# Performance work log

Hardware: AMD Instinct MI355X
Metric: run time of the kernel (lower is better)

## Reference

```python
import jax, jax.numpy as jnp
import numpy as np

B, P, ENC, DEC, EMB, ATT, V, L = 32, 196, 2048, 512, 512, 512, 32000, 21
T = L - 1  # decode steps


def setup_inputs() -> dict:
    key = jax.random.key(0)
    ks = jax.random.split(key, 20)
    u = lambda k, s, a=0.1: jax.random.uniform(k, s, jnp.float32, -a, a)
    lens = jax.random.randint(ks[1], (B, 1), 5, L + 1)
    lens = lens.at[0, 0].set(L)  # force max_decode_len == T (static)
    return {
        'encoder_out': jax.random.normal(ks[0], (B, P, ENC), jnp.float32),
        'encoded_captions': jax.random.randint(ks[2], (B, L), 0, V),
        'caption_lengths': lens,
        'emb_W': u(ks[3], (V, EMB)),
        'W_ea': u(ks[4], (ATT, ENC), 0.02), 'b_ea': jnp.zeros((ATT,)),
        'W_da': u(ks[5], (ATT, DEC), 0.02), 'b_da': jnp.zeros((ATT,)),
        'w_fa': u(ks[6], (1, ATT), 0.02), 'b_fa': jnp.zeros((1,)),
        'W_ih': u(ks[7], (4 * DEC, EMB + ENC), 0.02), 'b_ih': jnp.zeros((4 * DEC,)),
        'W_hh': u(ks[8], (4 * DEC, DEC), 0.02), 'b_hh': jnp.zeros((4 * DEC,)),
        'W_h0': u(ks[9], (DEC, ENC), 0.02), 'b_h0': jnp.zeros((DEC,)),
        'W_c0': u(ks[10], (DEC, ENC), 0.02), 'b_c0': jnp.zeros((DEC,)),
        'W_fb': u(ks[11], (ENC, DEC), 0.02), 'b_fb': jnp.zeros((ENC,)),
        'W_fc': u(ks[12], (V, DEC)), 'b_fc': jnp.zeros((V,)),
    }


def reference(encoder_out, encoded_captions, caption_lengths, emb_W,
              W_ea, b_ea, W_da, b_da, w_fa, b_fa,
              W_ih, b_ih, W_hh, b_hh, W_h0, b_h0, W_c0, b_c0,
              W_fb, b_fb, W_fc, b_fc):
    # sort by caption length descending (as in torch forward)
    lens = caption_lengths[:, 0]
    sort_ind = jnp.argsort(-lens)
    lens_s = lens[sort_ind]
    enc = encoder_out[sort_ind]          # [B,P,ENC]
    caps = encoded_captions[sort_ind]    # [B,L]
    dec_lens = lens_s - 1

    mean_enc = enc.mean(axis=1)
    h0 = mean_enc @ W_h0.T + b_h0
    c0 = mean_enc @ W_c0.T + b_c0

    att1 = jnp.einsum('bpe,ae->bpa', enc, W_ea) + b_ea  # precompute encoder attn proj
    embs = emb_W[caps]                                   # [B,L,EMB]
    emb_seq = jnp.transpose(embs[:, :T], (1, 0, 2))      # [T,B,EMB] (teacher forcing)
    mask_seq = jnp.arange(T)[:, None] < dec_lens[None, :]  # [T,B]

    def step(carry, xs):
        h, c = carry
        emb_t, m = xs  # [B,EMB], [B] bool; m emulates shrinking batch_size_t
        att2 = h @ W_da.T + b_da
        e = jnp.maximum(att1 + att2[:, None, :], 0.0) @ w_fa[0] + b_fa[0]  # [B,P]
        alpha = jax.nn.softmax(e, axis=1)
        awe = jnp.einsum('bp,bpe->be', alpha, enc)
        gate = jax.nn.sigmoid(h @ W_fb.T + b_fb)
        x = jnp.concatenate([emb_t, gate * awe], axis=1)
        g = x @ W_ih.T + b_ih + h @ W_hh.T + b_hh
        i, f, gg, o = jnp.split(g, 4, axis=1)
        c_new = jax.nn.sigmoid(f) * c + jax.nn.sigmoid(i) * jnp.tanh(gg)
        h_new = jax.nn.sigmoid(o) * jnp.tanh(c_new)
        preds = h_new @ W_fc.T + b_fc  # dropout in eval mode (identity)
        mf = m[:, None]
        h = jnp.where(mf, h_new, h)
        c = jnp.where(mf, c_new, c)
        preds = preds * mf.astype(preds.dtype)
        alpha = alpha * mf.astype(alpha.dtype)
        return (h, c), (preds, alpha)

    _, (preds, alphas) = jax.lax.scan(step, (h0, c0), (emb_seq, mask_seq))
    predictions = jnp.transpose(preds, (1, 0, 2))  # [B,T,V]
    alphas = jnp.transpose(alphas, (1, 0, 2))      # [B,T,P]
    return predictions, alphas
```

## Files before the change

### kernel.cpp

```cpp
#include <hip/hip_runtime.h>
#include <hip/hip_bf16.h>
#include <cstddef>

#define NB 32
#define NP 196
#define NE 2048
#define ND 512
#define NV 32000
#define NL 21
#define NT 20

typedef __attribute__((ext_vector_type(8))) short short8;
typedef __attribute__((ext_vector_type(4))) float f32x4;

__device__ __forceinline__ unsigned short f2b(float f) {
    __hip_bfloat16 h = __float2bfloat16(f);
    return *reinterpret_cast<unsigned short*>(&h);
}
__device__ __forceinline__ float b2f(unsigned short u) {
    union { unsigned int i; float f; } v; v.i = (unsigned)u << 16; return v.f;
}
__device__ __forceinline__ float b2f_lo(unsigned int u) {
    union { unsigned int i; float f; } v; v.i = u << 16; return v.f;
}
__device__ __forceinline__ float b2f_hi(unsigned int u) {
    union { unsigned int i; float f; } v; v.i = u & 0xffff0000u; return v.f;
}


__global__ void k_sort(const int* __restrict__ lens, int* __restrict__ sind, int* __restrict__ dlens,
                       int* __restrict__ rowmap, int* __restrict__ mpad)
{
    int i = threadIdx.x;
    if (i < NB) {
        int li = lens[i];
        int r = 0;
        for (int j = 0; j < NB; ++j) {
            int lj = lens[j];
            if (lj > li || (lj == li && j < i)) ++r;
        }
        sind[r] = i;
        dlens[r] = li - 1;
    }
    __syncthreads();
    if (i == 0) {
        int c = 0;
        for (int t = 0; t < NT; ++t)
            for (int b = 0; b < NB; ++b)
                if (t < dlens[b]) rowmap[c++] = t * NB + b;
        int pad = (c + 63) & ~63;
        for (int r = c; r < pad; ++r) rowmap[r] = -1;
        mpad[0] = pad;
    }
}

__global__ __launch_bounds__(256) void k_conv_enc(
    const float* __restrict__ enc, const int* __restrict__ sind,
    unsigned short* __restrict__ encB)
{
    int idx = (blockIdx.x * 256 + threadIdx.x) * 8;
    int b = idx / (NP * NE), rem = idx - b * (NP * NE);
    const float* src = enc + (size_t)sind[b] * NP * NE + rem;
    float4 a = *reinterpret_cast<const float4*>(src);
    float4 c = *reinterpret_cast<const float4*>(src + 4);
    uint4 o;
    o.x = f2b(a.x) | ((unsigned)f2b(a.y) << 16);
    o.y = f2b(a.z) | ((unsigned)f2b(a.w) << 16);
    o.z = f2b(c.x) | ((unsigned)f2b(c.y) << 16);
    o.w = f2b(c.z) | ((unsigned)f2b(c.w) << 16);
    *reinterpret_cast<uint4*>(encB + idx) = o;
}

__global__ __launch_bounds__(256) void k_emb(
    const int* __restrict__ caps, const int* __restrict__ sind,
    const float* __restrict__ emb_W, float* __restrict__ embS)
{
    int t = blockIdx.x, b = blockIdx.y;
    const float* src = emb_W + (size_t)caps[sind[b] * NL + t] * ND;
    float* dst = embS + ((size_t)t * NB + b) * ND;
    int i = threadIdx.x * 2;
    *reinterpret_cast<float2*>(dst + i) = *reinterpret_cast<const float2*>(src + i);
}

__global__ __launch_bounds__(256) void k_mean(const float* __restrict__ enc, const int* __restrict__ sind,
                                              float* __restrict__ mean_enc)
{
    int b = blockIdx.y;
    int k = blockIdx.x * 256 + threadIdx.x;
    const float* e = enc + (size_t)sind[b] * NP * NE + k;
    float s0 = 0.f, s1 = 0.f, s2 = 0.f, s3 = 0.f;
    for (int p = 0; p < NP; p += 4) {
        s0 += e[(size_t)(p + 0) * NE];
        s1 += e[(size_t)(p + 1) * NE];
        s2 += e[(size_t)(p + 2) * NE];
        s3 += e[(size_t)(p + 3) * NE];
    }
    mean_enc[(size_t)b * NE + k] = (s0 + s1 + s2 + s3) * (1.0f / NP);
}

__global__ __launch_bounds__(256) void k_zero(const int* __restrict__ dlens, float* __restrict__ out)
{
    int b = blockIdx.x / NT, t = blockIdx.x % NT;
    if (t < dlens[b]) return;
    float4 z = {0.f, 0.f, 0.f, 0.f};
    float4* row = (float4*)(out + ((size_t)b * NT + t) * NV);
    for (int i = threadIdx.x; i < NV / 4; i += 256) row[i] = z;
}

__device__ __forceinline__ void tile_body_uniW(
    const float* __restrict__ A, int lda, const float* __restrict__ W, int wstride,
    int n0, int kbeg, int kend, float* As, float (*Ws)[33], float acc[4][2],
    int tid)
{
    int lb = tid / 8, lkq = tid % 8;
    int b4 = (tid / 32) * 4, nl = (tid % 32) * 2;
    for (int kt = kbeg; kt < kend; kt += 32) {
        float4 a4 = *reinterpret_cast<const float4*>(A + (size_t)lb * lda + kt + lkq * 4);
        As[(lkq * 4 + 0) * 32 + lb] = a4.x; As[(lkq * 4 + 1) * 32 + lb] = a4.y;
        As[(lkq * 4 + 2) * 32 + lb] = a4.z; As[(lkq * 4 + 3) * 32 + lb] = a4.w;
        #pragma unroll
        for (int r = 0; r < 2; ++r) {
            int s = tid + r * 256;
            int n_l = s / 8, kq = s % 8;
            float4 w4 = *reinterpret_cast<const float4*>(W + (size_t)(n0 + n_l) * wstride + kt + kq * 4);
            Ws[n_l][kq * 4 + 0] = w4.x; Ws[n_l][kq * 4 + 1] = w4.y;
            Ws[n_l][kq * 4 + 2] = w4.z; Ws[n_l][kq * 4 + 3] = w4.w;
        }
        __syncthreads();
        #pragma unroll
        for (int k = 0; k < 32; ++k) {
            float4 av = *reinterpret_cast<const float4*>(&As[k * 32 + b4]);
            float w0 = Ws[nl][k], w1 = Ws[nl + 1][k];
            acc[0][0] += av.x * w0; acc[0][1] += av.x * w1;
            acc[1][0] += av.y * w0; acc[1][1] += av.y * w1;
            acc[2][0] += av.z * w0; acc[2][1] += av.z * w1;
            acc[3][0] += av.w * w0; acc[3][1] += av.w * w1;
        }
        __syncthreads();
    }
}

__global__ __launch_bounds__(256) void gemm_skinny_split(
    const float* __restrict__ A0, const float* __restrict__ W0a, const float* __restrict__ W0b,
    float* __restrict__ spart)
{
    __shared__ float As[1024];
    __shared__ float Ws[64][33];
    int n0 = blockIdx.x * 64;
    int ks = blockIdx.y;
    int tid = threadIdx.x;
    int lb = tid / 8, lkq = tid % 8;
    int b4 = (tid / 32) * 4, nl = (tid % 32) * 2;
    float acc[4][2] = {};
    for (int kt = ks * 256; kt < ks * 256 + 256; kt += 32) {
        float4 a4 = *reinterpret_cast<const float4*>(A0 + (size_t)lb * NE + kt + lkq * 4);
        As[(lkq * 4 + 0) * 32 + lb] = a4.x; As[(lkq * 4 + 1) * 32 + lb] = a4.y;
        As[(lkq * 4 + 2) * 32 + lb] = a4.z; As[(lkq * 4 + 3) * 32 + lb] = a4.w;
        #pragma unroll
        for (int r = 0; r < 2; ++r) {
            int s = tid + r * 256;
            int n_l = s / 8, kq = s % 8;
            int ng = n0 + n_l;
            const float* wrow = (ng < 512) ? (W0a + (size_t)ng * NE)
                                           : (W0b + (size_t)(ng - 512) * NE);
            float4 w4 = *reinterpret_cast<const float4*>(wrow + kt + kq * 4);
            Ws[n_l][kq * 4 + 0] = w4.x; Ws[n_l][kq * 4 + 1] = w4.y;
            Ws[n_l][kq * 4 + 2] = w4.z; Ws[n_l][kq * 4 + 3] = w4.w;
        }
        __syncthreads();
        #pragma unroll
        for (int k = 0; k < 32; ++k) {
            float4 av = *reinterpret_cast<const float4*>(&As[k * 32 + b4]);
            float w0 = Ws[nl][k], w1 = Ws[nl + 1][k];
            acc[0][0] += av.x * w0; acc[0][1] += av.x * w1;
            acc[1][0] += av.y * w0; acc[1][1] += av.y * w1;
            acc[2][0] += av.z * w0; acc[2][1] += av.z * w1;
            acc[3][0] += av.w * w0; acc[3][1] += av.w * w1;
        }
        __syncthreads();
    }
    float* Cp = spart + (size_t)ks * NB * 1024;
    #pragma unroll
    for (int j = 0; j < 2; ++j)
        #pragma unroll
        for (int i = 0; i < 4; ++i)
            Cp[(size_t)(b4 + i) * 1024 + n0 + nl + j] = acc[i][j];
}

__global__ __launch_bounds__(256) void k_hc0(
    const float* __restrict__ spart, const float* __restrict__ ba, const float* __restrict__ bb,
    float* __restrict__ hc)
{
    int b = blockIdx.x;
    for (int ng = threadIdx.x; ng < 1024; ng += 256) {
        float s = (ng < 512) ? ba[ng] : bb[ng - 512];
        #pragma unroll
        for (int ks = 0; ks < 8; ++ks)
            s += spart[(size_t)ks * NB * 1024 + (size_t)b * 1024 + ng];
        hc[(size_t)b * 1024 + ng] = s;
    }
}

__global__ __launch_bounds__(256) void gemm_att1_mfma(
    const float* __restrict__ enc, const float* __restrict__ W_ea,
    const float* __restrict__ bias, unsigned short* __restrict__ att1B,
    const int* __restrict__ sind)
{
    int fid = blockIdx.x;
    int c = fid & 7, x = (fid >> 3) & 7, pg = fid >> 6;
    int p = pg * 8 + c;
    if (p >= 98) return;
    int bm0 = p * 64, bn0 = x * 64;
    __shared__ unsigned short As[64][40];
    __shared__ unsigned short Bs[64][40];
    int tid = threadIdx.x;
    int w = tid >> 6, lane = tid & 63;
    int srow = tid >> 2, schunk = (tid & 3) * 8;
    int mg = bm0 + srow;
    int bidx = mg / NP, pp = mg - bidx * NP;
    const float* arow = enc + ((size_t)sind[bidx] * NP + pp) * NE + schunk;
    const float* brow = W_ea + (size_t)(bn0 + srow) * NE + schunk;
    int frow = lane & 15, fk = (lane >> 4) * 8;
    f32x4 acc[4] = {};
    for (int kt = 0; kt < NE; kt += 32) {
        float4 a0 = *reinterpret_cast<const float4*>(arow + kt);
        float4 a1 = *reinterpret_cast<const float4*>(arow + kt + 4);
        float4 b0 = *reinterpret_cast<const float4*>(brow + kt);
        float4 b1 = *reinterpret_cast<const float4*>(brow + kt + 4);
        uint4 av, bv;
        av.x = f2b(a0.x) | ((unsigned)f2b(a0.y) << 16);
        av.y = f2b(a0.z) | ((unsigned)f2b(a0.w) << 16);
        av.z = f2b(a1.x) | ((unsigned)f2b(a1.y) << 16);
        av.w = f2b(a1.z) | ((unsigned)f2b(a1.w) << 16);
        bv.x = f2b(b0.x) | ((unsigned)f2b(b0.y) << 16);
        bv.y = f2b(b0.z) | ((unsigned)f2b(b0.w) << 16);
        bv.z = f2b(b1.x) | ((unsigned)f2b(b1.y) << 16);
        bv.w = f2b(b1.z) | ((unsigned)f2b(b1.w) << 16);
        *reinterpret_cast<uint4*>(&As[srow][schunk]) = av;
        *reinterpret_cast<uint4*>(&Bs[srow][schunk]) = bv;
        __syncthreads();
        short8 af = *reinterpret_cast<const short8*>(&As[w * 16 + frow][fk]);
        #pragma unroll
        for (int n = 0; n < 4; ++n) {
            short8 bf = *reinterpret_cast<const short8*>(&Bs[n * 16 + frow][fk]);
            acc[n] = __builtin_amdgcn_mfma_f32_16x16x32_bf16(af, bf, acc[n], 0, 0, 0);
        }
        __syncthreads();
    }
    int crow = bm0 + w * 16 + (lane >> 4) * 4;
    int ccol0 = lane & 15;
    #pragma unroll
    for (int n = 0; n < 4; ++n) {
        int col = bn0 + n * 16 + ccol0;
        float bb2 = bias[col];
        #pragma unroll
        for (int i = 0; i < 4; ++i)
            att1B[(size_t)(crow + i) * ND + col] = f2b(acc[n][i] + bb2);
    }
}

__global__ __launch_bounds__(256) void gemm_preds_mfma(
    const unsigned short* __restrict__ hseqB, const float* __restrict__ W_fc,
    const float* __restrict__ bias, float* __restrict__ out,
    const int* __restrict__ rowmap, const int* __restrict__ mpad)
{
    int fid = blockIdx.x;
    int c = fid & 7;
    int rem = fid >> 3;
    int m = rem % 10, g = rem / 10;
    int n = g * 8 + c;
    if (n >= 250) return;
    int bm0 = m * 64;
    if (bm0 >= mpad[0]) return;
    int bn0 = n * 128;
    __shared__ unsigned short As[64][40];
    __shared__ unsigned short Bs[128][40];
    int tid = threadIdx.x;
    int w = tid >> 6, lane = tid & 63;
    int srow = tid >> 2, schunk = (tid & 3) * 8;
    int rid = rowmap[bm0 + srow];
    const unsigned short* aptr = hseqB + (size_t)(rid < 0 ? 0 : rid) * ND + schunk;
    const float* bptr0 = W_fc + (size_t)(bn0 + srow) * ND + schunk;
    const float* bptr1 = W_fc + (size_t)(bn0 + 64 + srow) * ND + schunk;
    int frow = lane & 15, fk = (lane >> 4) * 8;
    f32x4 acc[8] = {};
    for (int kt = 0; kt < ND; kt += 32) {
        uint4 av = *reinterpret_cast<const uint4*>(aptr + kt);
        float4 c0 = *reinterpret_cast<const float4*>(bptr0 + kt);
        float4 c1 = *reinterpret_cast<const float4*>(bptr0 + kt + 4);
        float4 d0 = *reinterpret_cast<const float4*>(bptr1 + kt);
        float4 d1 = *reinterpret_cast<const float4*>(bptr1 + kt + 4);
        uint4 bv0, bv1;
        bv0.x = f2b(c0.x) | ((unsigned)f2b(c0.y) << 16);
        bv0.y = f2b(c0.z) | ((unsigned)f2b(c0.w) << 16);
        bv0.z = f2b(c1.x) | ((unsigned)f2b(c1.y) << 16);
        bv0.w = f2b(c1.z) | ((unsigned)f2b(c1.w) << 16);
        bv1.x = f2b(d0.x) | ((unsigned)f2b(d0.y) << 16);
        bv1.y = f2b(d0.z) | ((unsigned)f2b(d0.w) << 16);
        bv1.z = f2b(d1.x) | ((unsigned)f2b(d1.y) << 16);
        bv1.w = f2b(d1.z) | ((unsigned)f2b(d1.w) << 16);
        *reinterpret_cast<uint4*>(&As[srow][schunk]) = av;
        *reinterpret_cast<uint4*>(&Bs[srow][schunk]) = bv0;
        *reinterpret_cast<uint4*>(&Bs[64 + srow][schunk]) = bv1;
        __syncthreads();
        short8 af = *reinterpret_cast<const short8*>(&As[w * 16 + frow][fk]);
        #pragma unroll
        for (int nn = 0; nn < 8; ++nn) {
            short8 bf = *reinterpret_cast<const short8*>(&Bs[nn * 16 + frow][fk]);
            acc[nn] = __builtin_amdgcn_mfma_f32_16x16x32_bf16(af, bf, acc[nn], 0, 0, 0);
        }
        __syncthreads();
    }
    int rl0 = w * 16 + (lane >> 4) * 4;
    int ccol0 = lane & 15;
    #pragma unroll
    for (int i = 0; i < 4; ++i) {
        int rm = rowmap[bm0 + rl0 + i];
        if (rm < 0) continue;
        int t = rm / NB, b = rm % NB;
        float* orow = out + ((size_t)b * NT + t) * NV;
        #pragma unroll
        for (int nn = 0; nn < 8; ++nn) {
            int col = bn0 + nn * 16 + ccol0;
            orow[col] = acc[nn][i] + bias[col];
        }
    }
}

__global__ __launch_bounds__(256) void k_phase1(
    const float* __restrict__ hc, const float* __restrict__ W_da, const float* __restrict__ W_fb,
    const float* __restrict__ b_da, const float* __restrict__ b_fb,
    const float* __restrict__ embS, const float* __restrict__ W_ih, const float* __restrict__ W_hh,
    float* __restrict__ attg, float* __restrict__ gpart, int t)
{
    __shared__ float As[1024];
    __shared__ float Ws[64][33];
    int blk = blockIdx.x, tid = threadIdx.x;
    int b4 = (tid / 32) * 4, nl = (tid % 32) * 2;
    float acc[4][2] = {};
    if (blk < 40) {
        int n0 = blk * 64;
        int lb = tid / 8, lkq = tid % 8;
        for (int kt = 0; kt < 512; kt += 32) {
            float4 a4 = *reinterpret_cast<const float4*>(hc + (size_t)lb * 1024 + kt + lkq * 4);
            As[(lkq * 4 + 0) * 32 + lb] = a4.x; As[(lkq * 4 + 1) * 32 + lb] = a4.y;
            As[(lkq * 4 + 2) * 32 + lb] = a4.z; As[(lkq * 4 + 3) * 32 + lb] = a4.w;
            #pragma unroll
            for (int r = 0; r < 2; ++r) {
                int s = tid + r * 256;
                int n_l = s / 8, kq = s % 8;
                int ng = n0 + n_l;
                const float* wrow = (ng < 512) ? (W_da + (size_t)ng * 512)
                                               : (W_fb + (size_t)(ng - 512) * 512);
                float4 w4 = *reinterpret_cast<const float4*>(wrow + kt + kq * 4);
                Ws[n_l][kq * 4 + 0] = w4.x; Ws[n_l][kq * 4 + 1] = w4.y;
                Ws[n_l][kq * 4 + 2] = w4.z; Ws[n_l][kq * 4 + 3] = w4.w;
            }
            __syncthreads();
            #pragma unroll
            for (int k = 0; k < 32; ++k) {
                float4 av = *reinterpret_cast<const float4*>(&As[k * 32 + b4]);
                float w0 = Ws[nl][k], w1 = Ws[nl + 1][k];
                acc[0][0] += av.x * w0; acc[0][1] += av.x * w1;
                acc[1][0] += av.y * w0; acc[1][1] += av.y * w1;
                acc[2][0] += av.z * w0; acc[2][1] += av.z * w1;
                acc[3][0] += av.w * w0; acc[3][1] += av.w * w1;
            }
            __syncthreads();
        }
        #pragma unroll
        for (int j = 0; j < 2; ++j) {
            int ng = n0 + nl + j;
            float bias = (ng < 512) ? b_da[ng] : b_fb[ng - 512];
            #pragma unroll
            for (int i = 0; i < 4; ++i)
                attg[(size_t)(b4 + i) * 2560 + ng] = acc[i][j] + bias;
        }
    } else if (blk < 72) {
        int nt = blk - 40, n0 = nt * 64;
        tile_body_uniW(embS + (size_t)t * NB * ND, ND, W_ih, 2560, n0, 0, 512, As, Ws, acc, tid);
        float* Cp = gpart + (size_t)4 * NB * 2048;
        #pragma unroll
        for (int j = 0; j < 2; ++j)
            #pragma unroll
            for (int i = 0; i < 4; ++i)
                Cp[(size_t)(b4 + i) * 2048 + n0 + nl + j] = acc[i][j];
    } else {
        int nt = blk - 72, n0 = nt * 64;
        tile_body_uniW(hc, 1024, W_hh, 512, n0, 0, 512, As, Ws, acc, tid);
        float* Cp = gpart + (size_t)5 * NB * 2048;
        #pragma unroll
        for (int j = 0; j < 2; ++j)
            #pragma unroll
            for (int i = 0; i < 4; ++i)
                Cp[(size_t)(b4 + i) * 2048 + n0 + nl + j] = acc[i][j];
    }
}

__global__ __launch_bounds__(256) void k_e(
    const unsigned short* __restrict__ att1B, const float* __restrict__ attg,
    const float* __restrict__ w_fa, const float* __restrict__ b_fa,
    float* __restrict__ e)
{
    __shared__ float att2s[ND];
    __shared__ float wfas[ND];
    int b = blockIdx.y, tid = threadIdx.x;
    const float* ag = attg + (size_t)b * 2560;
    for (int d = tid; d < ND; d += 256) { att2s[d] = ag[d]; wfas[d] = w_fa[d]; }
    __syncthreads();
    int w = tid >> 6, lane = tid & 63;
    int p0 = blockIdx.x * 28;
    const unsigned short* a1 = att1B + ((size_t)b * NP + p0) * ND;
    #pragma unroll
    for (int i = 0; i < 7; ++i) {
        int p = w + 4 * i;
        const unsigned short* row = a1 + (size_t)p * ND;
        float s = 0.f;
        #pragma unroll
        for (int j = 0; j < 2; ++j) {
            int d = j * 256 + lane * 4;
            uint2 u = *reinterpret_cast<const uint2*>(row + d);
            float v0 = b2f_lo(u.x), v1 = b2f_hi(u.x);
            float v2 = b2f_lo(u.y), v3 = b2f_hi(u.y);
            float4 a2 = *reinterpret_cast<const float4*>(&att2s[d]);
            float4 wf = *reinterpret_cast<const float4*>(&wfas[d]);
            s += fmaxf(v0 + a2.x, 0.f) * wf.x + fmaxf(v1 + a2.y, 0.f) * wf.y
               + fmaxf(v2 + a2.z, 0.f) * wf.z + fmaxf(v3 + a2.w, 0.f) * wf.w;
        }
        for (int off = 32; off > 0; off >>= 1) s += __shfl_down(s, off);
        if (lane == 0) e[(size_t)b * NP + p0 + p] = s + b_fa[0];
    }
}

__global__ __launch_bounds__(256) void k_awe(
    const unsigned short* __restrict__ encB, const int* __restrict__ dlens,
    const float* __restrict__ e, const float* __restrict__ attg,
    float* __restrict__ xh, float* __restrict__ out_alpha, int t)
{
    __shared__ float es[256];
    __shared__ float red[256];
    int kc = blockIdx.x, b = blockIdx.y, tid = threadIdx.x;
    float ev = -1e30f;
    if (tid < NP) { float v = e[(size_t)b * NP + tid]; es[tid] = v; ev = v; }
    red[tid] = ev; __syncthreads();
    for (int s2 = 128; s2 > 0; s2 >>= 1) { if (tid < s2) red[tid] = fmaxf(red[tid], red[tid + s2]); __syncthreads(); }
    float m = red[0]; __syncthreads();
    float xe = (tid < NP) ? expf(es[tid] - m) : 0.f;
    red[tid] = xe; __syncthreads();
    for (int s2 = 128; s2 > 0; s2 >>= 1) { if (tid < s2) red[tid] += red[tid + s2]; __syncthreads(); }
    float inv = 1.0f / red[0];
    __syncthreads();
    es[tid] = xe * inv;
    __syncthreads();

    int k = kc * 256 + tid;
    const unsigned short* ec = encB + (size_t)b * NP * NE + k;
    float s0 = 0.f, s1 = 0.f, s2v = 0.f, s3 = 0.f;
    #pragma unroll 4
    for (int p = 0; p < NP; p += 4) {
        s0 += es[p + 0] * b2f(ec[(size_t)(p + 0) * NE]);
        s1 += es[p + 1] * b2f(ec[(size_t)(p + 1) * NE]);
        s2v += es[p + 2] * b2f(ec[(size_t)(p + 2) * NE]);
        s3 += es[p + 3] * b2f(ec[(size_t)(p + 3) * NE]);
    }
    float awe = (s0 + s1) + (s2v + s3);
    float gp = attg[(size_t)b * 2560 + 512 + k];
    float gate = 1.f / (1.f + expf(-gp));
    xh[(size_t)b * 3072 + 512 + k] = gate * awe;
    if (kc == 0 && tid < NP) {
        bool live = (t < dlens[b]);
        out_alpha[((size_t)b * NT + t) * NP + tid] = live ? es[tid] : 0.f;
    }
}

__global__ __launch_bounds__(256) void k_gates(
    const float* __restrict__ xh, const float* __restrict__ W_ih,
    float* __restrict__ gpart)
{
    __shared__ float As[1024];
    __shared__ float Ws[64][33];
    int blk = blockIdx.x, tid = threadIdx.x;
    int nt = blk & 31, ks = blk >> 5;
    int n0 = nt * 64;
    int b4 = (tid / 32) * 4, nl = (tid % 32) * 2;
    float acc[4][2] = {};
    tile_body_uniW(xh + 512 + (size_t)ks * 512, 3072, W_ih + 512 + (size_t)ks * 512, 2560,
                   n0, 0, 512, As, Ws, acc, tid);
    float* Cp = gpart + (size_t)ks * NB * 2048;
    #pragma unroll
    for (int j = 0; j < 2; ++j)
        #pragma unroll
        for (int i = 0; i < 4; ++i)
            Cp[(size_t)(b4 + i) * 2048 + n0 + nl + j] = acc[i][j];
}

__global__ __launch_bounds__(256) void k_cell(
    const float* __restrict__ gpart, const int* __restrict__ dlens,
    const float* __restrict__ b_ih, const float* __restrict__ b_hh,
    float* __restrict__ hc, unsigned short* __restrict__ hseqB, int t)
{
    int b = blockIdx.x;
    for (int d = threadIdx.x; d < ND; d += 256) {
        float g0 = b_ih[d] + b_hh[d];
        float g1 = b_ih[512 + d] + b_hh[512 + d];
        float g2 = b_ih[1024 + d] + b_hh[1024 + d];
        float g3 = b_ih[1536 + d] + b_hh[1536 + d];
        #pragma unroll
        for (int ks = 0; ks < 6; ++ks) {
            const float* gp = gpart + ((size_t)ks * NB + b) * 2048;
            g0 += gp[d]; g1 += gp[512 + d]; g2 += gp[1024 + d]; g3 += gp[1536 + d];
        }
        float ig = 1.f / (1.f + expf(-g0));
        float fg = 1.f / (1.f + expf(-g1));
        float gt = tanhf(g2);
        float og = 1.f / (1.f + expf(-g3));
        float c_old = hc[(size_t)b * 1024 + 512 + d];
        float c_new = fg * c_old + ig * gt;
        float h_new = og * tanhf(c_new);
        hseqB[((size_t)t * NB + b) * ND + d] = f2b(h_new);
        if (t < dlens[b]) {
            hc[(size_t)b * 1024 + d] = h_new;
            hc[(size_t)b * 1024 + 512 + d] = c_new;
        }
    }
}

extern "C" void kernel_launch(void* const* d_in, const int* in_sizes, int n_in,
                              void* d_out, int out_size, void* d_ws, size_t ws_size,
                              hipStream_t stream)
{
    const float* enc   = (const float*)d_in[0];
    const int*   caps  = (const int*)d_in[1];
    const int*   clens = (const int*)d_in[2];
    const float* emb_W = (const float*)d_in[3];
    const float* W_ea  = (const float*)d_in[4];
    const float* b_ea  = (const float*)d_in[5];
    const float* W_da  = (const float*)d_in[6];
    const float* b_da  = (const float*)d_in[7];
    const float* w_fa  = (const float*)d_in[8];
    const float* b_fa  = (const float*)d_in[9];
    const float* W_ih  = (const float*)d_in[10];
    const float* b_ih  = (const float*)d_in[11];
    const float* W_hh  = (const float*)d_in[12];
    const float* b_hh  = (const float*)d_in[13];
    const float* W_h0  = (const float*)d_in[14];
    const float* b_h0  = (const float*)d_in[15];
    const float* W_c0  = (const float*)d_in[16];
    const float* b_c0  = (const float*)d_in[17];
    const float* W_fb  = (const float*)d_in[18];
    const float* b_fb  = (const float*)d_in[19];
    const float* W_fc  = (const float*)d_in[20];
    const float* b_fc  = (const float*)d_in[21];

    float* out = (float*)d_out;
    float* out_alpha = out + (size_t)NB * NT * NV;

    int* iws    = (int*)d_ws;
    int* sind   = iws;
    int* dlens  = iws + 32;
    int* rowmap = iws + 64;
    int* mpad   = iws + 704;
    float* base = (float*)d_ws + 1024;
    float* mean_enc = base;
    float* hc    = mean_enc + NB * NE;
    float* attg  = hc + NB * 1024;
    float* xh    = attg + NB * 2560;
    float* e     = xh + NB * 3072;
    float* embS  = e + NB * NP;
    float* gpart = embS + (size_t)NT * NB * ND;
    unsigned short* att1B = (unsigned short*)(gpart + 6 * NB * 2048);
    unsigned short* hseqB = att1B + (size_t)NB * NP * ND;
    unsigned short* encB  = hseqB + (size_t)NT * NB * ND;

    k_sort<<<1, 64, 0, stream>>>(clens, sind, dlens, rowmap, mpad);
    k_zero<<<NB * NT, 256, 0, stream>>>(dlens, out);
    k_conv_enc<<<dim3(NB * NP * NE / 2048), 256, 0, stream>>>(enc, sind, encB);
    k_emb<<<dim3(NT, NB), 256, 0, stream>>>(caps, sind, emb_W, embS);
    k_mean<<<dim3(NE / 256, NB), 256, 0, stream>>>(enc, sind, mean_enc);
    gemm_skinny_split<<<dim3(16, 8), 256, 0, stream>>>(mean_enc, W_h0, W_c0, gpart);
    k_hc0<<<dim3(NB), 256, 0, stream>>>(gpart, b_h0, b_c0, hc);
    gemm_att1_mfma<<<dim3(832), 256, 0, stream>>>(enc, W_ea, b_ea, att1B, sind);

    for (int t = 0; t < NT; ++t) {
        k_phase1<<<dim3(104), 256, 0, stream>>>(hc, W_da, W_fb, b_da, b_fb,
                                                embS, W_ih, W_hh, attg, gpart, t);
        k_e<<<dim3(7, NB), 256, 0, stream>>>(att1B, attg, w_fa, b_fa, e);
        k_awe<<<dim3(8, NB), 256, 0, stream>>>(encB, dlens, e, attg, xh, out_alpha, t);
        k_gates<<<dim3(128), 256, 0, stream>>>(xh, W_ih, gpart);
        k_cell<<<dim3(NB), 256, 0, stream>>>(gpart, dlens, b_ih, b_hh, hc, hseqB, t);
    }

    gemm_preds_mfma<<<dim3(2560), 256, 0, stream>>>(hseqB, W_fc, b_fc, out, rowmap, mpad);
}
```

Measured before the change: 1.580 ms.

## Fuse gate GEMM with LSTM cell and enlarge prediction GEMM row tile

New measurement: 2.232 ms. +41.3%, slower.

```diff
diff --git a/kernel.cpp b/kernel.cpp
--- a/kernel.cpp
+++ b/kernel.cpp
@@ -48,7 +48,7 @@
         for (int t = 0; t < NT; ++t)
             for (int b = 0; b < NB; ++b)
                 if (t < dlens[b]) rowmap[c++] = t * NB + b;
-        int pad = (c + 63) & ~63;
+        int pad = (c + 127) & ~127;
         for (int r = c; r < pad; ++r) rowmap[r] = -1;
         mpad[0] = pad;
     }
@@ -267,62 +267,69 @@
     int fid = blockIdx.x;
     int c = fid & 7;
     int rem = fid >> 3;
-    int m = rem % 10, g = rem / 10;
+    int m = rem % 5, g = rem / 5;
     int n = g * 8 + c;
     if (n >= 250) return;
-    int bm0 = m * 64;
+    int bm0 = m * 128;
     if (bm0 >= mpad[0]) return;
     int bn0 = n * 128;
-    __shared__ unsigned short As[64][40];
+    __shared__ unsigned short As[128][40];
     __shared__ unsigned short Bs[128][40];
     int tid = threadIdx.x;
     int w = tid >> 6, lane = tid & 63;
-    int srow = tid >> 2, schunk = (tid & 3) * 8;
+    int srow = tid >> 1, shalf = (tid & 1) * 16;
     int rid = rowmap[bm0 + srow];
-    const unsigned short* aptr = hseqB + (size_t)(rid < 0 ? 0 : rid) * ND + schunk;
-    const float* bptr0 = W_fc + (size_t)(bn0 + srow) * ND + schunk;
-    const float* bptr1 = W_fc + (size_t)(bn0 + 64 + srow) * ND + schunk;
+    const unsigned short* aptr = hseqB + (size_t)(rid < 0 ? 0 : rid) * ND + shalf;
+    const float* bptr = W_fc + (size_t)(bn0 + srow) * ND + shalf;
     int frow = lane & 15, fk = (lane >> 4) * 8;
-    f32x4 acc[8] = {};
+    f32x4 acc[2][8] = {};
     for (int kt = 0; kt < ND; kt += 32) {
-        uint4 av = *reinterpret_cast<const uint4*>(aptr + kt);
-        float4 c0 = *reinterpret_cast<const float4*>(bptr0 + kt);
-        float4 c1 = *reinterpret_cast<const float4*>(bptr0 + kt + 4);
-        float4 d0 = *reinterpret_cast<const float4*>(bptr1 + kt);
-        float4 d1 = *reinterpret_cast<const float4*>(bptr1 + kt + 4);
+        uint4 a0 = *reinterpret_cast<const uint4*>(aptr + kt);
+        uint4 a1 = *reinterpret_cast<const uint4*>(aptr + kt + 8);
+        float4 c0 = *reinterpret_cast<const float4*>(bptr + kt);
+        float4 c1 = *reinterpret_cast<const float4*>(bptr + kt + 4);
+        float4 c2 = *reinterpret_cast<const float4*>(bptr + kt + 8);
+        float4 c3 = *reinterpret_cast<const float4*>(bptr + kt + 12);
         uint4 bv0, bv1;
         bv0.x = f2b(c0.x) | ((unsigned)f2b(c0.y) << 16);
         bv0.y = f2b(c0.z) | ((unsigned)f2b(c0.w) << 16);
         bv0.z = f2b(c1.x) | ((unsigned)f2b(c1.y) << 16);
         bv0.w = f2b(c1.z) | ((unsigned)f2b(c1.w) << 16);
-        bv1.x = f2b(d0.x) | ((unsigned)f2b(d0.y) << 16);
-        bv1.y = f2b(d0.z) | ((unsigned)f2b(d0.w) << 16);
-        bv1.z = f2b(d1.x) | ((unsigned)f2b(d1.y) << 16);
-        bv1.w = f2b(d1.z) | ((unsigned)f2b(d1.w) << 16);
-        *reinterpret_cast<uint4*>(&As[srow][schunk]) = av;
-        *reinterpret_cast<uint4*>(&Bs[srow][schunk]) = bv0;
-        *reinterpret_cast<uint4*>(&Bs[64 + srow][schunk]) = bv1;
-        __syncthreads();
-        short8 af = *reinterpret_cast<const short8*>(&As[w * 16 + frow][fk]);
-        #pragma unroll
-        for (int nn = 0; nn < 8; ++nn) {
-            short8 bf = *reinterpret_cast<const short8*>(&Bs[nn * 16 + frow][fk]);
-            acc[nn] = __builtin_amdgcn_mfma_f32_16x16x32_bf16(af, bf, acc[nn], 0, 0, 0);
-        }
-        __syncthreads();
-    }
-    int rl0 = w * 16 + (lane >> 4) * 4;
+        bv1.x = f2b(c2.x) | ((unsigned)f2b(c2.y) << 16);
+        bv1.y = f2b(c2.z) | ((unsigned)f2b(c2.w) << 16);
+        bv1.z = f2b(c3.x) | ((unsigned)f2b(c3.y) << 16);
+        bv1.w = f2b(c3.z) | ((unsigned)f2b(c3.w) << 16);
+        *reinterpret_cast<uint4*>(&As[srow][shalf]) = a0;
+        *reinterpret_cast<uint4*>(&As[srow][shalf + 8]) = a1;
+        *reinterpret_cast<uint4*>(&Bs[srow][shalf]) = bv0;
+        *reinterpret_cast<uint4*>(&Bs[srow][shalf + 8]) = bv1;
+        __syncthreads();
+        #pragma unroll
+        for (int h = 0; h < 2; ++h) {
+            short8 af = *reinterpret_cast<const short8*>(&As[w * 32 + h * 16 + frow][fk]);
+            #pragma unroll
+            for (int nn = 0; nn < 8; ++nn) {
+                short8 bf = *reinterpret_cast<const short8*>(&Bs[nn * 16 + frow][fk]);
+                acc[h][nn] = __builtin_amdgcn_mfma_f32_16x16x32_bf16(af, bf, acc[h][nn], 0, 0, 0);
+            }
+        }
+        __syncthreads();
+    }
     int ccol0 = lane & 15;
     #pragma unroll
-    for (int i = 0; i < 4; ++i) {
-        int rm = rowmap[bm0 + rl0 + i];
-        if (rm < 0) continue;
-        int t = rm / NB, b = rm % NB;
-        float* orow = out + ((size_t)b * NT + t) * NV;
-        #pragma unroll
-        for (int nn = 0; nn < 8; ++nn) {
-            int col = bn0 + nn * 16 + ccol0;
-            orow[col] = acc[nn][i] + bias[col];
+    for (int h = 0; h < 2; ++h) {
+        int rl0 = w * 32 + h * 16 + (lane >> 4) * 4;
+        #pragma unroll
+        for (int i = 0; i < 4; ++i) {
+            int rm = rowmap[bm0 + rl0 + i];
+            if (rm < 0) continue;
+            int t = rm / NB, b = rm % NB;
+            float* orow = out + ((size_t)b * NT + t) * NV;
+            #pragma unroll
+            for (int nn = 0; nn < 8; ++nn) {
+                int col = bn0 + nn * 16 + ccol0;
+                orow[col] = acc[h][nn][i] + bias[col];
+            }
         }
     }
 }
@@ -473,47 +480,57 @@
     }
 }
 
-__global__ __launch_bounds__(256) void k_gates(
+__global__ __launch_bounds__(256) void k_gatescell(
     const float* __restrict__ xh, const float* __restrict__ W_ih,
-    float* __restrict__ gpart)
-{
-    __shared__ float As[1024];
-    __shared__ float Ws[64][33];
-    int blk = blockIdx.x, tid = threadIdx.x;
-    int nt = blk & 31, ks = blk >> 5;
-    int n0 = nt * 64;
-    int b4 = (tid / 32) * 4, nl = (tid % 32) * 2;
-    float acc[4][2] = {};
-    tile_body_uniW(xh + 512 + (size_t)ks * 512, 3072, W_ih + 512 + (size_t)ks * 512, 2560,
-                   n0, 0, 512, As, Ws, acc, tid);
-    float* Cp = gpart + (size_t)ks * NB * 2048;
-    #pragma unroll
-    for (int j = 0; j < 2; ++j)
-        #pragma unroll
-        for (int i = 0; i < 4; ++i)
-            Cp[(size_t)(b4 + i) * 2048 + n0 + nl + j] = acc[i][j];
-}
-
-__global__ __launch_bounds__(256) void k_cell(
     const float* __restrict__ gpart, const int* __restrict__ dlens,
     const float* __restrict__ b_ih, const float* __restrict__ b_hh,
     float* __restrict__ hc, unsigned short* __restrict__ hseqB, int t)
 {
-    int b = blockIdx.x;
-    for (int d = threadIdx.x; d < ND; d += 256) {
-        float g0 = b_ih[d] + b_hh[d];
-        float g1 = b_ih[512 + d] + b_hh[512 + d];
-        float g2 = b_ih[1024 + d] + b_hh[1024 + d];
-        float g3 = b_ih[1536 + d] + b_hh[1536 + d];
-        #pragma unroll
-        for (int ks = 0; ks < 6; ++ks) {
-            const float* gp = gpart + ((size_t)ks * NB + b) * 2048;
-            g0 += gp[d]; g1 += gp[512 + d]; g2 += gp[1024 + d]; g3 += gp[1536 + d];
-        }
-        float ig = 1.f / (1.f + expf(-g0));
-        float fg = 1.f / (1.f + expf(-g1));
-        float gt = tanhf(g2);
-        float og = 1.f / (1.f + expf(-g3));
+    __shared__ float As[1024];
+    __shared__ float Ws[16][33];
+    __shared__ float Gs[512];
+    int dc = blockIdx.x, tid = threadIdx.x;
+    int lb = tid / 8, lkq = tid % 8;
+    int wr = tid >> 4, wk = (tid & 15) * 2;
+    int grow = (wr >> 2) * 512 + dc * 4 + (wr & 3);
+    const float* wrow = W_ih + (size_t)grow * 2560 + 512;
+    int r = tid & 15, bp = tid >> 4;
+    int b0 = bp * 2;
+    float acc0 = 0.f, acc1 = 0.f;
+    for (int kt = 0; kt < 2048; kt += 32) {
+        float4 a4 = *reinterpret_cast<const float4*>(xh + (size_t)lb * 3072 + 512 + kt + lkq * 4);
+        As[(lkq * 4 + 0) * 32 + lb] = a4.x; As[(lkq * 4 + 1) * 32 + lb] = a4.y;
+        As[(lkq * 4 + 2) * 32 + lb] = a4.z; As[(lkq * 4 + 3) * 32 + lb] = a4.w;
+        float2 w2 = *reinterpret_cast<const float2*>(wrow + kt + wk);
+        Ws[wr][wk] = w2.x; Ws[wr][wk + 1] = w2.y;
+        __syncthreads();
+        #pragma unroll
+        for (int k = 0; k < 32; ++k) {
+            float wv = Ws[r][k];
+            float2 av = *reinterpret_cast<const float2*>(&As[k * 32 + b0]);
+            acc0 += av.x * wv;
+            acc1 += av.y * wv;
+        }
+        __syncthreads();
+    }
+    Gs[r * 32 + b0] = acc0;
+    Gs[r * 32 + b0 + 1] = acc1;
+    __syncthreads();
+    if (tid < 128) {
+        int d_l = tid & 3, b = tid >> 2;
+        int d = dc * 4 + d_l;
+        const float* gp4 = gpart + ((size_t)4 * NB + b) * 2048;
+        const float* gp5 = gpart + ((size_t)5 * NB + b) * 2048;
+        float g[4];
+        #pragma unroll
+        for (int q = 0; q < 4; ++q) {
+            int n = q * 512 + d;
+            g[q] = Gs[(q * 4 + d_l) * 32 + b] + gp4[n] + gp5[n] + b_ih[n] + b_hh[n];
+        }
+        float ig = 1.f / (1.f + expf(-g[0]));
+        float fg = 1.f / (1.f + expf(-g[1]));
+        float gt = tanhf(g[2]);
+        float og = 1.f / (1.f + expf(-g[3]));
         float c_old = hc[(size_t)b * 1024 + 512 + d];
         float c_new = fg * c_old + ig * gt;
         float h_new = og * tanhf(c_new);
@@ -586,9 +603,9 @@
                                                 embS, W_ih, W_hh, attg, gpart, t);
         k_e<<<dim3(7, NB), 256, 0, stream>>>(att1B, attg, w_fa, b_fa, e);
         k_awe<<<dim3(8, NB), 256, 0, stream>>>(encB, dlens, e, attg, xh, out_alpha, t);
-        k_gates<<<dim3(128), 256, 0, stream>>>(xh, W_ih, gpart);
-        k_cell<<<dim3(NB), 256, 0, stream>>>(gpart, dlens, b_ih, b_hh, hc, hseqB, t);
-    }
-
-    gemm_preds_mfma<<<dim3(2560), 256, 0, stream>>>(hseqB, W_fc, b_fc, out, rowmap, mpad);
-}
+        k_gatescell<<<dim3(128), 256, 0, stream>>>(xh, W_ih, gpart, dlens,
+                                                   b_ih, b_hh, hc, hseqB, t);
+    }
+
+    gemm_preds_mfma<<<dim3(1280), 256, 0, stream>>>(hseqB, W_fc, b_fc, out, rowmap, mpad);
+}
```
